# Optimization experiments

Hardware: AMD Instinct MI355X
Metric: run time of the kernel (lower is better)

## Reference

```python
import jax, jax.numpy as jnp
import numpy as np

B, S, D_IN, D_OUT = 4, 2048, 1024, 1024

def setup_inputs() -> dict:
    key = jax.random.key(0)
    k1, k2, k3, k4 = jax.random.split(key, 4)
    x = jax.random.normal(k1, (B, S, D_IN), dtype=jnp.float32)
    # nn.Linear weights: [out, in]; y = x @ W.T
    scale = 1.0 / np.sqrt(D_IN)
    W_key = jax.random.uniform(k2, (D_OUT, D_IN), dtype=jnp.float32, minval=-scale, maxval=scale)
    W_query = jax.random.uniform(k3, (D_OUT, D_IN), dtype=jnp.float32, minval=-scale, maxval=scale)
    W_value = jax.random.uniform(k4, (D_OUT, D_IN), dtype=jnp.float32, minval=-scale, maxval=scale)
    return {"x": x, "W_key": W_key, "W_query": W_query, "W_value": W_value}

def reference(x, W_key, W_query, W_value):
    # x: [B, S, D_IN]; W_*: [D_OUT, D_IN]
    keys = jnp.einsum('bsd,od->bso', x, W_key)
    queries = jnp.einsum('bsd,od->bso', x, W_query)
    values = jnp.einsum('bsd,od->bso', x, W_value)
    # attn_scores: [B, S, S]
    scores = jnp.einsum('bqo,bko->bqk', queries, keys)
    inv_sqrt_d = 1.0 / jnp.sqrt(jnp.asarray(keys.shape[-1], dtype=scores.dtype))
    weights = jax.nn.softmax(scores * inv_sqrt_d, axis=-1)
    context = jnp.einsum('bqk,bko->bqo', weights, values)
    return context
```

## Files before the change

kernel.cpp:

```cpp
#include <hip/hip_runtime.h>

typedef unsigned short u16;
typedef __attribute__((ext_vector_type(4))) float f32x4;
typedef __attribute__((ext_vector_type(8))) short bf16x8;
typedef __attribute__((ext_vector_type(4))) u16 u16x4;
typedef __attribute__((ext_vector_type(8))) u16 u16x8;

__device__ __forceinline__ u16 f2bf(float f) {
    unsigned u = __float_as_uint(f);
    unsigned r = (u + 0x7FFFu + ((u >> 16) & 1u)) >> 16;
    return (u16)r;
}

__device__ __forceinline__ void gld16(const void* g, void* l) {
    __builtin_amdgcn_global_load_lds(
        (const __attribute__((address_space(1))) unsigned*)g,
        (__attribute__((address_space(3))) unsigned*)l,
        16, 0, 0);
}

__global__ __launch_bounds__(256) void cast_kernel(const float* __restrict__ in,
                                                   u16* __restrict__ out, int n4) {
    int i = blockIdx.x * blockDim.x + threadIdx.x;
    int stride = gridDim.x * blockDim.x;
    for (; i < n4; i += stride) {
        f32x4 v = ((const f32x4*)in)[i];
        u16x4 o;
        o[0] = f2bf(v[0]); o[1] = f2bf(v[1]); o[2] = f2bf(v[2]); o[3] = f2bf(v[3]);
        ((u16x4*)out)[i] = o;
    }
}

__global__ __launch_bounds__(256) void zero_kernel(float* __restrict__ p, int n) {
    int i = blockIdx.x * blockDim.x + threadIdx.x;
    if (i < n) p[i] = 0.f;
}

template <int EPI>
__global__ __launch_bounds__(512, 1) void gemm256(
    const u16* __restrict__ A, const u16* __restrict__ Bm, void* __restrict__ Cv,
    int K, int lda, int ldb, int ldc,
    long long sA, long long sB, long long sC, float scale,
    float* __restrict__ denom) {
    extern __shared__ char smem[];
    const u16* Ab = A + (long long)blockIdx.z * sA;
    const u16* Bb = Bm + (long long)blockIdx.z * sB;

    const int tid  = threadIdx.x;
    const int lane = tid & 63;
    const int w    = tid >> 6;
    const int wm   = w >> 2;
    const int wn   = w & 3;
    const int rowBase = blockIdx.x << 8;
    const int colBase = blockIdx.y << 8;
    const int NT = K >> 6;
    const int aRow = lane & 15;

    auto stage = [&](int tile, int h) {
        if (tile >= NT) return;
        const int db = tile & 1;
        const int kt = tile << 6;
        const u16* mat; int ldm, rb, halfRow; char* region;
        if (h == 0)      { mat = Ab; ldm = lda; rb = rowBase; halfRow = 0;   region = smem + db * 32768; }
        else if (h == 1) { mat = Bb; ldm = ldb; rb = colBase; halfRow = 0;   region = smem + 65536 + db * 32768; }
        else if (h == 2) { mat = Bb; ldm = ldb; rb = colBase; halfRow = 128; region = smem + 65536 + db * 32768; }
        else             { mat = Ab; ldm = lda; rb = rowBase; halfRow = 128; region = smem + db * 32768; }
#pragma unroll
        for (int i = 0; i < 2; i++) {
            int o    = ((i * 8 + w) << 10) + lane * 16;
            int r    = o >> 7;
            int slot = (o >> 4) & 7;
            const u16* g = mat + (size_t)(rb + halfRow + r) * ldm + kt +
                           ((slot ^ (r & 7)) << 3);
            gld16(g, region + halfRow * 128 + ((i * 8 + w) << 10));
        }
    };
    auto ldA = [&](int db, int row, int ks) -> bf16x8 {
        int byte = db * 32768 + row * 128 + ((((ks << 2) | (lane >> 4)) ^ (row & 7)) << 4);
        return *(const bf16x8*)(smem + byte);
    };
    auto ldB = [&](int db, int row, int ks) -> bf16x8 {
        int byte = 65536 + db * 32768 + row * 128 + ((((ks << 2) | (lane >> 4)) ^ (row & 7)) << 4);
        return *(const bf16x8*)(smem + byte);
    };

    f32x4 acc[8][4] = {};
    bf16x8 aF[4][2], b0[2][2], b1[2][2];

    stage(0, 0); stage(0, 3); stage(0, 1); stage(0, 2);
    stage(1, 1); stage(1, 2);
    __builtin_amdgcn_sched_barrier(0);
    asm volatile("s_waitcnt vmcnt(4)" ::: "memory");
    __builtin_amdgcn_sched_barrier(0);
    __builtin_amdgcn_s_barrier();

    for (int t = 0; t < NT; ++t) {
        const int db = t & 1;
#pragma unroll
        for (int m = 0; m < 4; m++)
#pragma unroll
            for (int ks = 0; ks < 2; ks++)
                aF[m][ks] = ldA(db, wm * 128 + m * 16 + aRow, ks);
#pragma unroll
        for (int n = 0; n < 2; n++)
#pragma unroll
            for (int ks = 0; ks < 2; ks++)
                b0[n][ks] = ldB(db, wn * 64 + n * 16 + aRow, ks);
        stage(t + 1, 0);
        __builtin_amdgcn_s_barrier();
        asm volatile("s_waitcnt lgkmcnt(0)" ::: "memory");
        __builtin_amdgcn_sched_barrier(0);
        __builtin_amdgcn_s_setprio(1);
#pragma unroll
        for (int ks = 0; ks < 2; ks++)
#pragma unroll
            for (int m = 0; m < 4; m++)
#pragma unroll
                for (int n = 0; n < 2; n++)
                    acc[m][n] = __builtin_amdgcn_mfma_f32_16x16x32_bf16(
                        aF[m][ks], b0[n][ks], acc[m][n], 0, 0, 0);
        __builtin_amdgcn_s_setprio(0);
#pragma unroll
        for (int n = 0; n < 2; n++)
#pragma unroll
            for (int ks = 0; ks < 2; ks++)
                b1[n][ks] = ldB(db, wn * 64 + (n + 2) * 16 + aRow, ks);
        stage(t + 1, 3);
        __builtin_amdgcn_s_barrier();
        asm volatile("s_waitcnt lgkmcnt(0)" ::: "memory");
        __builtin_amdgcn_sched_barrier(0);
        __builtin_amdgcn_s_setprio(1);
#pragma unroll
        for (int ks = 0; ks < 2; ks++)
#pragma unroll
            for (int m = 0; m < 4; m++)
#pragma unroll
                for (int n = 0; n < 2; n++)
                    acc[m][n + 2] = __builtin_amdgcn_mfma_f32_16x16x32_bf16(
                        aF[m][ks], b1[n][ks], acc[m][n + 2], 0, 0, 0);
        __builtin_amdgcn_s_setprio(0);
#pragma unroll
        for (int m = 0; m < 4; m++)
#pragma unroll
            for (int ks = 0; ks < 2; ks++)
                aF[m][ks] = ldA(db, wm * 128 + (m + 4) * 16 + aRow, ks);
        __builtin_amdgcn_s_barrier();
        asm volatile("s_waitcnt lgkmcnt(0)" ::: "memory");
        __builtin_amdgcn_sched_barrier(0);
        __builtin_amdgcn_s_setprio(1);
#pragma unroll
        for (int ks = 0; ks < 2; ks++)
#pragma unroll
            for (int m = 0; m < 4; m++)
#pragma unroll
                for (int n = 0; n < 2; n++)
                    acc[m + 4][n + 2] = __builtin_amdgcn_mfma_f32_16x16x32_bf16(
                        aF[m][ks], b1[n][ks], acc[m + 4][n + 2], 0, 0, 0);
        __builtin_amdgcn_s_setprio(0);
        stage(t + 2, 1);
        stage(t + 2, 2);
        __builtin_amdgcn_sched_barrier(0);
        if (t + 2 < NT) { asm volatile("s_waitcnt vmcnt(4)" ::: "memory"); }
        else            { asm volatile("s_waitcnt vmcnt(0)" ::: "memory"); }
        __builtin_amdgcn_sched_barrier(0);
        __builtin_amdgcn_s_barrier();
        __builtin_amdgcn_s_setprio(1);
#pragma unroll
        for (int ks = 0; ks < 2; ks++)
#pragma unroll
            for (int m = 0; m < 4; m++)
#pragma unroll
                for (int n = 0; n < 2; n++)
                    acc[m + 4][n] = __builtin_amdgcn_mfma_f32_16x16x32_bf16(
                        aF[m][ks], b0[n][ks], acc[m + 4][n], 0, 0, 0);
        __builtin_amdgcn_s_setprio(0);
    }

    const int row0 = rowBase + wm * 128 + ((lane >> 4) << 2);
    const int col0 = colBase + wn * 64 + (lane & 15);
    long long cb = (long long)blockIdx.z * sC;
    if (EPI == 0) {
#pragma unroll
        for (int m = 0; m < 8; m++)
#pragma unroll
            for (int n = 0; n < 4; n++) {
                f32x4 v = acc[m][n];
#pragma unroll
                for (int j = 0; j < 4; j++) {
                    size_t idx = (size_t)(row0 + m * 16 + j) * ldc + (col0 + n * 16);
                    ((u16*)Cv)[cb + idx] = f2bf(v[j] * scale);
                }
            }
    } else {
        float* dz = denom + (long long)blockIdx.z * 2048;
#pragma unroll
        for (int m = 0; m < 8; m++) {
#pragma unroll
            for (int j = 0; j < 4; j++) {
                const int row = row0 + m * 16 + j;
                float rs = 0.f;
#pragma unroll
                for (int n = 0; n < 4; n++) {
                    float e = __expf(fminf(acc[m][n][j] * scale, 60.f));
                    rs += e;
                    ((u16*)Cv)[cb + (size_t)row * ldc + (col0 + n * 16)] = f2bf(e);
                }
#pragma unroll
                for (int off = 1; off < 16; off <<= 1) rs += __shfl_xor(rs, off);
                if ((lane & 15) == 0) atomicAdd(&dz[row], rs);
            }
        }
    }
}

template <int EPI>
__global__ __launch_bounds__(512, 1) void gemm256n128(
    const u16* __restrict__ A, const u16* __restrict__ Bm, void* __restrict__ Cv,
    int K, int lda, int ldb, int ldc,
    long long sA, long long sB, long long sC, float scale,
    const float* __restrict__ denom) {
    extern __shared__ char smem[];
    const u16* Ab = A + (long long)blockIdx.z * sA;
    const u16* Bb = Bm + (long long)blockIdx.z * sB;

    const int tid  = threadIdx.x;
    const int lane = tid & 63;
    const int w    = tid >> 6;
    const int wm   = w >> 1;
    const int wn   = w & 1;
    const int rowBase = blockIdx.x << 8;
    const int colBase = blockIdx.y << 7;
    const int NT = K >> 6;
    const int aRow = lane & 15;

    auto stage = [&](int tile, int h) {
        if (tile >= NT) return;
        const int db = tile & 1;
        const int kt = tile << 6;
        if (h == 0 || h == 3) {
            const int halfRow = (h == 0) ? 0 : 128;
            char* region = smem + db * 32768;
#pragma unroll
            for (int i = 0; i < 2; i++) {
                int o    = i * 8192 + tid * 16;
                int r    = o >> 7;
                int slot = (o >> 4) & 7;
                const u16* g = Ab + (size_t)(rowBase + halfRow + r) * lda + kt +
                               ((slot ^ (r & 7)) << 3);
                gld16(g, region + halfRow * 128 + i * 8192 + (w << 10));
            }
        } else {
            const int halfRow = (h == 1) ? 0 : 64;
            char* region = smem + 65536 + db * 16384;
            int o    = tid * 16;
            int r    = o >> 7;
            int slot = (o >> 4) & 7;
            const u16* g = Bb + (size_t)(colBase + halfRow + r) * ldb + kt +
                           ((slot ^ (r & 7)) << 3);
            gld16(g, region + halfRow * 128 + (w << 10));
        }
    };
    auto ldA = [&](int db, int row, int ks) -> bf16x8 {
        int byte = db * 32768 + row * 128 + ((((ks << 2) | (lane >> 4)) ^ (row & 7)) << 4);
        return *(const bf16x8*)(smem + byte);
    };
    auto ldB = [&](int db, int row, int ks) -> bf16x8 {
        int byte = 65536 + db * 16384 + row * 128 + ((((ks << 2) | (lane >> 4)) ^ (row & 7)) << 4);
        return *(const bf16x8*)(smem + byte);
    };

    f32x4 acc[4][4] = {};
    bf16x8 aF[2][2], b0[2][2], b1[2][2];

    stage(0, 0); stage(0, 3); stage(0, 1); stage(0, 2);
    stage(1, 1); stage(1, 2);
    __builtin_amdgcn_sched_barrier(0);
    asm volatile("s_waitcnt vmcnt(2)" ::: "memory");
    __builtin_amdgcn_sched_barrier(0);
    __builtin_amdgcn_s_barrier();

    for (int t = 0; t < NT; ++t) {
        const int db = t & 1;
#pragma unroll
        for (int m = 0; m < 2; m++)
#pragma unroll
            for (int ks = 0; ks < 2; ks++)
                aF[m][ks] = ldA(db, wm * 64 + m * 16 + aRow, ks);
#pragma unroll
        for (int n = 0; n < 2; n++)
#pragma unroll
            for (int ks = 0; ks < 2; ks++)
                b0[n][ks] = ldB(db, wn * 64 + n * 16 + aRow, ks);
        stage(t + 1, 0);
        __builtin_amdgcn_s_barrier();
        asm volatile("s_waitcnt lgkmcnt(0)" ::: "memory");
        __builtin_amdgcn_sched_barrier(0);
        __builtin_amdgcn_s_setprio(1);
#pragma unroll
        for (int ks = 0; ks < 2; ks++)
#pragma unroll
            for (int m = 0; m < 2; m++)
#pragma unroll
                for (int n = 0; n < 2; n++)
                    acc[m][n] = __builtin_amdgcn_mfma_f32_16x16x32_bf16(
                        aF[m][ks], b0[n][ks], acc[m][n], 0, 0, 0);
        __builtin_amdgcn_s_setprio(0);
#pragma unroll
        for (int n = 0; n < 2; n++)
#pragma unroll
            for (int ks = 0; ks < 2; ks++)
                b1[n][ks] = ldB(db, wn * 64 + (n + 2) * 16 + aRow, ks);
        stage(t + 1, 3);
        __builtin_amdgcn_s_barrier();
        asm volatile("s_waitcnt lgkmcnt(0)" ::: "memory");
        __builtin_amdgcn_sched_barrier(0);
        __builtin_amdgcn_s_setprio(1);
#pragma unroll
        for (int ks = 0; ks < 2; ks++)
#pragma unroll
            for (int m = 0; m < 2; m++)
#pragma unroll
                for (int n = 0; n < 2; n++)
                    acc[m][n + 2] = __builtin_amdgcn_mfma_f32_16x16x32_bf16(
                        aF[m][ks], b1[n][ks], acc[m][n + 2], 0, 0, 0);
        __builtin_amdgcn_s_setprio(0);
#pragma unroll
        for (int m = 0; m < 2; m++)
#pragma unroll
            for (int ks = 0; ks < 2; ks++)
                aF[m][ks] = ldA(db, wm * 64 + (m + 2) * 16 + aRow, ks);
        __builtin_amdgcn_s_barrier();
        asm volatile("s_waitcnt lgkmcnt(0)" ::: "memory");
        __builtin_amdgcn_sched_barrier(0);
        __builtin_amdgcn_s_setprio(1);
#pragma unroll
        for (int ks = 0; ks < 2; ks++)
#pragma unroll
            for (int m = 0; m < 2; m++)
#pragma unroll
                for (int n = 0; n < 2; n++)
                    acc[m + 2][n + 2] = __builtin_amdgcn_mfma_f32_16x16x32_bf16(
                        aF[m][ks], b1[n][ks], acc[m + 2][n + 2], 0, 0, 0);
        __builtin_amdgcn_s_setprio(0);
        stage(t + 2, 1);
        stage(t + 2, 2);
        __builtin_amdgcn_sched_barrier(0);
        if (t + 2 < NT) { asm volatile("s_waitcnt vmcnt(2)" ::: "memory"); }
        else            { asm volatile("s_waitcnt vmcnt(0)" ::: "memory"); }
        __builtin_amdgcn_sched_barrier(0);
        __builtin_amdgcn_s_barrier();
        __builtin_amdgcn_s_setprio(1);
#pragma unroll
        for (int ks = 0; ks < 2; ks++)
#pragma unroll
            for (int m = 0; m < 2; m++)
#pragma unroll
                for (int n = 0; n < 2; n++)
                    acc[m + 2][n] = __builtin_amdgcn_mfma_f32_16x16x32_bf16(
                        aF[m][ks], b0[n][ks], acc[m + 2][n], 0, 0, 0);
        __builtin_amdgcn_s_setprio(0);
    }

    const int row0 = rowBase + wm * 64 + ((lane >> 4) << 2);
    const int col0 = colBase + wn * 64 + (lane & 15);
    long long cb = (long long)blockIdx.z * sC;
    if (EPI == 0) {
#pragma unroll
        for (int m = 0; m < 4; m++)
#pragma unroll
            for (int n = 0; n < 4; n++) {
                f32x4 v = acc[m][n];
#pragma unroll
                for (int j = 0; j < 4; j++) {
                    size_t idx = (size_t)(row0 + m * 16 + j) * ldc + (col0 + n * 16);
                    ((u16*)Cv)[cb + idx] = f2bf(v[j] * scale);
                }
            }
    } else {
        const float* dz = denom + (long long)blockIdx.z * 2048;
        float inv[4][4];
#pragma unroll
        for (int m = 0; m < 4; m++)
#pragma unroll
            for (int j = 0; j < 4; j++)
                inv[m][j] = 1.0f / dz[row0 + m * 16 + j];
#pragma unroll
        for (int m = 0; m < 4; m++)
#pragma unroll
            for (int n = 0; n < 4; n++) {
                f32x4 v = acc[m][n];
#pragma unroll
                for (int j = 0; j < 4; j++) {
                    size_t idx = (size_t)(row0 + m * 16 + j) * ldc + (col0 + n * 16);
                    ((float*)Cv)[cb + idx] = v[j] * inv[m][j];
                }
            }
    }
}

extern "C" void kernel_launch(void* const* d_in, const int* in_sizes, int n_in,
                              void* d_out, int out_size, void* d_ws, size_t ws_size,
                              hipStream_t stream) {
    const float* x  = (const float*)d_in[0];
    const float* Wk = (const float*)d_in[1];
    const float* Wq = (const float*)d_in[2];
    const float* Wv = (const float*)d_in[3];
    float* out = (float*)d_out;
    char* ws = (char*)d_ws;
    const size_t MB = 1u << 20;

    u16* xb    = (u16*)(ws);
    u16* Wqk   = (u16*)(ws + 16 * MB);
    u16* Wvb   = (u16*)(ws + 20 * MB);
    float* den = (float*)(ws + 22 * MB);
    u16* QK    = (u16*)(ws + 64 * MB);
    u16* VT    = (u16*)(ws + 96 * MB);
    u16* Pb    = (u16*)(ws + 112 * MB);

    const long long SS = 2048LL * 2048;

    hipFuncSetAttribute((const void*)gemm256<0>, hipFuncAttributeMaxDynamicSharedMemorySize, 131072);
    hipFuncSetAttribute((const void*)gemm256<2>, hipFuncAttributeMaxDynamicSharedMemorySize, 131072);
    hipFuncSetAttribute((const void*)gemm256n128<0>, hipFuncAttributeMaxDynamicSharedMemorySize, 98304);
    hipFuncSetAttribute((const void*)gemm256n128<3>, hipFuncAttributeMaxDynamicSharedMemorySize, 98304);

    cast_kernel<<<2048, 256, 0, stream>>>(x, xb, 8388608 / 4);
    cast_kernel<<<1024, 256, 0, stream>>>(Wq, Wqk, 1048576 / 4);
    cast_kernel<<<1024, 256, 0, stream>>>(Wk, Wqk + 1048576, 1048576 / 4);
    cast_kernel<<<1024, 256, 0, stream>>>(Wv, Wvb, 1048576 / 4);
    zero_kernel<<<32, 256, 0, stream>>>(den, 8192);

    gemm256<0><<<dim3(32, 8, 1), 512, 131072, stream>>>(
        xb, Wqk, QK, 1024, 1024, 1024, 2048, 0, 0, 0, 1.0f, nullptr);
    gemm256n128<0><<<dim3(4, 64, 1), 512, 98304, stream>>>(
        Wvb, xb, VT, 1024, 1024, 1024, 8192, 0, 0, 0, 1.0f, nullptr);
    gemm256<2><<<dim3(8, 8, 4), 512, 131072, stream>>>(
        QK, QK + 1024, Pb, 1024, 2048, 2048, 2048, SS, SS, SS, 0.03125f, den);
    gemm256n128<3><<<dim3(8, 8, 4), 512, 98304, stream>>>(
        Pb, VT, out, 2048, 2048, 8192, 1024, SS, 2048LL, 2048LL * 1024, 1.0f, den);
}
```

Baseline: 156.8 us.

## Software-pipeline LDS fragment loads across MFMA quadrants with separate register sets

```diff
diff --git a/kernel.cpp b/kernel.cpp
--- a/kernel.cpp
+++ b/kernel.cpp
@@ -85,7 +85,7 @@
     };
 
     f32x4 acc[8][4] = {};
-    bf16x8 aF[4][2], b0[2][2], b1[2][2];
+    bf16x8 a01[4][2], a23[4][2], b01[2][2], b23[2][2];
 
     stage(0, 0); stage(0, 3); stage(0, 1); stage(0, 2);
     stage(1, 1); stage(1, 2);
@@ -93,20 +93,56 @@
     asm volatile("s_waitcnt vmcnt(4)" ::: "memory");
     __builtin_amdgcn_sched_barrier(0);
     __builtin_amdgcn_s_barrier();
+#pragma unroll
+    for (int m = 0; m < 4; m++)
+#pragma unroll
+        for (int ks = 0; ks < 2; ks++)
+            a01[m][ks] = ldA(0, wm * 128 + m * 16 + aRow, ks);
+#pragma unroll
+    for (int n = 0; n < 2; n++)
+#pragma unroll
+        for (int ks = 0; ks < 2; ks++)
+            b01[n][ks] = ldB(0, wn * 64 + n * 16 + aRow, ks);
 
     for (int t = 0; t < NT; ++t) {
         const int db = t & 1;
 #pragma unroll
+        for (int n = 0; n < 2; n++)
+#pragma unroll
+            for (int ks = 0; ks < 2; ks++)
+                b23[n][ks] = ldB(db, wn * 64 + (n + 2) * 16 + aRow, ks);
+        stage(t + 1, 0);
+        asm volatile("s_waitcnt lgkmcnt(4)" ::: "memory");
+        __builtin_amdgcn_sched_barrier(0);
+        __builtin_amdgcn_s_setprio(1);
+#pragma unroll
+        for (int ks = 0; ks < 2; ks++)
+#pragma unroll
+            for (int m = 0; m < 4; m++)
+#pragma unroll
+                for (int n = 0; n < 2; n++)
+                    acc[m][n] = __builtin_amdgcn_mfma_f32_16x16x32_bf16(
+                        a01[m][ks], b01[n][ks], acc[m][n], 0, 0, 0);
+        __builtin_amdgcn_s_setprio(0);
+        __builtin_amdgcn_s_barrier();
+#pragma unroll
         for (int m = 0; m < 4; m++)
 #pragma unroll
             for (int ks = 0; ks < 2; ks++)
-                aF[m][ks] = ldA(db, wm * 128 + m * 16 + aRow, ks);
-#pragma unroll
-        for (int n = 0; n < 2; n++)
-#pragma unroll
-            for (int ks = 0; ks < 2; ks++)
-                b0[n][ks] = ldB(db, wn * 64 + n * 16 + aRow, ks);
-        stage(t + 1, 0);
+                a23[m][ks] = ldA(db, wm * 128 + (m + 4) * 16 + aRow, ks);
+        stage(t + 1, 3);
+        asm volatile("s_waitcnt lgkmcnt(8)" ::: "memory");
+        __builtin_amdgcn_sched_barrier(0);
+        __builtin_amdgcn_s_setprio(1);
+#pragma unroll
+        for (int ks = 0; ks < 2; ks++)
+#pragma unroll
+            for (int m = 0; m < 4; m++)
+#pragma unroll
+                for (int n = 0; n < 2; n++)
+                    acc[m][n + 2] = __builtin_amdgcn_mfma_f32_16x16x32_bf16(
+                        a01[m][ks], b23[n][ks], acc[m][n + 2], 0, 0, 0);
+        __builtin_amdgcn_s_setprio(0);
         __builtin_amdgcn_s_barrier();
         asm volatile("s_waitcnt lgkmcnt(0)" ::: "memory");
         __builtin_amdgcn_sched_barrier(0);
@@ -117,46 +153,10 @@
             for (int m = 0; m < 4; m++)
 #pragma unroll
                 for (int n = 0; n < 2; n++)
-                    acc[m][n] = __builtin_amdgcn_mfma_f32_16x16x32_bf16(
-                        aF[m][ks], b0[n][ks], acc[m][n], 0, 0, 0);
-        __builtin_amdgcn_s_setprio(0);
-#pragma unroll
-        for (int n = 0; n < 2; n++)
-#pragma unroll
-            for (int ks = 0; ks < 2; ks++)
-                b1[n][ks] = ldB(db, wn * 64 + (n + 2) * 16 + aRow, ks);
-        stage(t + 1, 3);
-        __builtin_amdgcn_s_barrier();
-        asm volatile("s_waitcnt lgkmcnt(0)" ::: "memory");
-        __builtin_amdgcn_sched_barrier(0);
-        __builtin_amdgcn_s_setprio(1);
-#pragma unroll
-        for (int ks = 0; ks < 2; ks++)
-#pragma unroll
-            for (int m = 0; m < 4; m++)
-#pragma unroll
-                for (int n = 0; n < 2; n++)
-                    acc[m][n + 2] = __builtin_amdgcn_mfma_f32_16x16x32_bf16(
-                        aF[m][ks], b1[n][ks], acc[m][n + 2], 0, 0, 0);
-        __builtin_amdgcn_s_setprio(0);
-#pragma unroll
-        for (int m = 0; m < 4; m++)
-#pragma unroll
-            for (int ks = 0; ks < 2; ks++)
-                aF[m][ks] = ldA(db, wm * 128 + (m + 4) * 16 + aRow, ks);
-        __builtin_amdgcn_s_barrier();
-        asm volatile("s_waitcnt lgkmcnt(0)" ::: "memory");
-        __builtin_amdgcn_sched_barrier(0);
-        __builtin_amdgcn_s_setprio(1);
-#pragma unroll
-        for (int ks = 0; ks < 2; ks++)
-#pragma unroll
-            for (int m = 0; m < 4; m++)
-#pragma unroll
-                for (int n = 0; n < 2; n++)
-                    acc[m + 4][n + 2] = __builtin_amdgcn_mfma_f32_16x16x32_bf16(
-                        aF[m][ks], b1[n][ks], acc[m + 4][n + 2], 0, 0, 0);
-        __builtin_amdgcn_s_setprio(0);
+                    acc[m + 4][n] = __builtin_amdgcn_mfma_f32_16x16x32_bf16(
+                        a23[m][ks], b01[n][ks], acc[m + 4][n], 0, 0, 0);
+        __builtin_amdgcn_s_setprio(0);
+        __builtin_amdgcn_s_barrier();
         stage(t + 2, 1);
         stage(t + 2, 2);
         __builtin_amdgcn_sched_barrier(0);
@@ -164,15 +164,28 @@
         else            { asm volatile("s_waitcnt vmcnt(0)" ::: "memory"); }
         __builtin_amdgcn_sched_barrier(0);
         __builtin_amdgcn_s_barrier();
-        __builtin_amdgcn_s_setprio(1);
-#pragma unroll
-        for (int ks = 0; ks < 2; ks++)
+        if (t + 1 < NT) {
 #pragma unroll
             for (int m = 0; m < 4; m++)
 #pragma unroll
-                for (int n = 0; n < 2; n++)
-                    acc[m + 4][n] = __builtin_amdgcn_mfma_f32_16x16x32_bf16(
-                        aF[m][ks], b0[n][ks], acc[m + 4][n], 0, 0, 0);
+                for (int ks = 0; ks < 2; ks++)
+                    a01[m][ks] = ldA(db ^ 1, wm * 128 + m * 16 + aRow, ks);
+#pragma unroll
+            for (int n = 0; n < 2; n++)
+#pragma unroll
+                for (int ks = 0; ks < 2; ks++)
+                    b01[n][ks] = ldB(db ^ 1, wn * 64 + n * 16 + aRow, ks);
+        }
+        __builtin_amdgcn_sched_barrier(0);
+        __builtin_amdgcn_s_setprio(1);
+#pragma unroll
+        for (int ks = 0; ks < 2; ks++)
+#pragma unroll
+            for (int m = 0; m < 4; m++)
+#pragma unroll
+                for (int n = 0; n < 2; n++)
+                    acc[m + 4][n + 2] = __builtin_amdgcn_mfma_f32_16x16x32_bf16(
+                        a23[m][ks], b23[n][ks], acc[m + 4][n + 2], 0, 0, 0);
         __builtin_amdgcn_s_setprio(0);
     }
 
@@ -270,7 +283,7 @@
     };
 
     f32x4 acc[4][4] = {};
-    bf16x8 aF[2][2], b0[2][2], b1[2][2];
+    bf16x8 a01[2][2], a23[2][2], b01[2][2], b23[2][2];
 
     stage(0, 0); stage(0, 3); stage(0, 1); stage(0, 2);
     stage(1, 1); stage(1, 2);
@@ -278,20 +291,56 @@
     asm volatile("s_waitcnt vmcnt(2)" ::: "memory");
     __builtin_amdgcn_sched_barrier(0);
     __builtin_amdgcn_s_barrier();
+#pragma unroll
+    for (int m = 0; m < 2; m++)
+#pragma unroll
+        for (int ks = 0; ks < 2; ks++)
+            a01[m][ks] = ldA(0, wm * 64 + m * 16 + aRow, ks);
+#pragma unroll
+    for (int n = 0; n < 2; n++)
+#pragma unroll
+        for (int ks = 0; ks < 2; ks++)
+            b01[n][ks] = ldB(0, wn * 64 + n * 16 + aRow, ks);
 
     for (int t = 0; t < NT; ++t) {
         const int db = t & 1;
 #pragma unroll
+        for (int n = 0; n < 2; n++)
+#pragma unroll
+            for (int ks = 0; ks < 2; ks++)
+                b23[n][ks] = ldB(db, wn * 64 + (n + 2) * 16 + aRow, ks);
+        stage(t + 1, 0);
+        asm volatile("s_waitcnt lgkmcnt(4)" ::: "memory");
+        __builtin_amdgcn_sched_barrier(0);
+        __builtin_amdgcn_s_setprio(1);
+#pragma unroll
+        for (int ks = 0; ks < 2; ks++)
+#pragma unroll
+            for (int m = 0; m < 2; m++)
+#pragma unroll
+                for (int n = 0; n < 2; n++)
+                    acc[m][n] = __builtin_amdgcn_mfma_f32_16x16x32_bf16(
+                        a01[m][ks], b01[n][ks], acc[m][n], 0, 0, 0);
+        __builtin_amdgcn_s_setprio(0);
+        __builtin_amdgcn_s_barrier();
+#pragma unroll
         for (int m = 0; m < 2; m++)
 #pragma unroll
             for (int ks = 0; ks < 2; ks++)
-                aF[m][ks] = ldA(db, wm * 64 + m * 16 + aRow, ks);
-#pragma unroll
-        for (int n = 0; n < 2; n++)
-#pragma unroll
-            for (int ks = 0; ks < 2; ks++)
-                b0[n][ks] = ldB(db, wn * 64 + n * 16 + aRow, ks);
-        stage(t + 1, 0);
+                a23[m][ks] = ldA(db, wm * 64 + (m + 2) * 16 + aRow, ks);
+        stage(t + 1, 3);
+        asm volatile("s_waitcnt lgkmcnt(4)" ::: "memory");
+        __builtin_amdgcn_sched_barrier(0);
+        __builtin_amdgcn_s_setprio(1);
+#pragma unroll
+        for (int ks = 0; ks < 2; ks++)
+#pragma unroll
+            for (int m = 0; m < 2; m++)
+#pragma unroll
+                for (int n = 0; n < 2; n++)
+                    acc[m][n + 2] = __builtin_amdgcn_mfma_f32_16x16x32_bf16(
+                        a01[m][ks], b23[n][ks], acc[m][n + 2], 0, 0, 0);
+        __builtin_amdgcn_s_setprio(0);
         __builtin_amdgcn_s_barrier();
         asm volatile("s_waitcnt lgkmcnt(0)" ::: "memory");
         __builtin_amdgcn_sched_barrier(0);
@@ -302,46 +351,10 @@
             for (int m = 0; m < 2; m++)
 #pragma unroll
                 for (int n = 0; n < 2; n++)
-                    acc[m][n] = __builtin_amdgcn_mfma_f32_16x16x32_bf16(
-                        aF[m][ks], b0[n][ks], acc[m][n], 0, 0, 0);
-        __builtin_amdgcn_s_setprio(0);
-#pragma unroll
-        for (int n = 0; n < 2; n++)
-#pragma unroll
-            for (int ks = 0; ks < 2; ks++)
-                b1[n][ks] = ldB(db, wn * 64 + (n + 2) * 16 + aRow, ks);
-        stage(t + 1, 3);
-        __builtin_amdgcn_s_barrier();
-        asm volatile("s_waitcnt lgkmcnt(0)" ::: "memory");
-        __builtin_amdgcn_sched_barrier(0);
-        __builtin_amdgcn_s_setprio(1);
-#pragma unroll
-        for (int ks = 0; ks < 2; ks++)
-#pragma unroll
-            for (int m = 0; m < 2; m++)
-#pragma unroll
-                for (int n = 0; n < 2; n++)
-                    acc[m][n + 2] = __builtin_amdgcn_mfma_f32_16x16x32_bf16(
-                        aF[m][ks], b1[n][ks], acc[m][n + 2], 0, 0, 0);
-        __builtin_amdgcn_s_setprio(0);
-#pragma unroll
-        for (int m = 0; m < 2; m++)
-#pragma unroll
-            for (int ks = 0; ks < 2; ks++)
-                aF[m][ks] = ldA(db, wm * 64 + (m + 2) * 16 + aRow, ks);
-        __builtin_amdgcn_s_barrier();
-        asm volatile("s_waitcnt lgkmcnt(0)" ::: "memory");
-        __builtin_amdgcn_sched_barrier(0);
-        __builtin_amdgcn_s_setprio(1);
-#pragma unroll
-        for (int ks = 0; ks < 2; ks++)
-#pragma unroll
-            for (int m = 0; m < 2; m++)
-#pragma unroll
-                for (int n = 0; n < 2; n++)
-                    acc[m + 2][n + 2] = __builtin_amdgcn_mfma_f32_16x16x32_bf16(
-                        aF[m][ks], b1[n][ks], acc[m + 2][n + 2], 0, 0, 0);
-        __builtin_amdgcn_s_setprio(0);
+                    acc[m + 2][n] = __builtin_amdgcn_mfma_f32_16x16x32_bf16(
+                        a23[m][ks], b01[n][ks], acc[m + 2][n], 0, 0, 0);
+        __builtin_amdgcn_s_setprio(0);
+        __builtin_amdgcn_s_barrier();
         stage(t + 2, 1);
         stage(t + 2, 2);
         __builtin_amdgcn_sched_barrier(0);
@@ -349,15 +362,28 @@
         else            { asm volatile("s_waitcnt vmcnt(0)" ::: "memory"); }
         __builtin_amdgcn_sched_barrier(0);
         __builtin_amdgcn_s_barrier();
-        __builtin_amdgcn_s_setprio(1);
-#pragma unroll
-        for (int ks = 0; ks < 2; ks++)
+        if (t + 1 < NT) {
 #pragma unroll
             for (int m = 0; m < 2; m++)
 #pragma unroll
-                for (int n = 0; n < 2; n++)
-                    acc[m + 2][n] = __builtin_amdgcn_mfma_f32_16x16x32_bf16(
-                        aF[m][ks], b0[n][ks], acc[m + 2][n], 0, 0, 0);
+                for (int ks = 0; ks < 2; ks++)
+                    a01[m][ks] = ldA(db ^ 1, wm * 64 + m * 16 + aRow, ks);
+#pragma unroll
+            for (int n = 0; n < 2; n++)
+#pragma unroll
+                for (int ks = 0; ks < 2; ks++)
+                    b01[n][ks] = ldB(db ^ 1, wn * 64 + n * 16 + aRow, ks);
+        }
+        __builtin_amdgcn_sched_barrier(0);
+        __builtin_amdgcn_s_setprio(1);
+#pragma unroll
+        for (int ks = 0; ks < 2; ks++)
+#pragma unroll
+            for (int m = 0; m < 2; m++)
+#pragma unroll
+                for (int n = 0; n < 2; n++)
+                    acc[m + 2][n + 2] = __builtin_amdgcn_mfma_f32_16x16x32_bf16(
+                        a23[m][ks], b23[n][ks], acc[m + 2][n + 2], 0, 0, 0);
         __builtin_amdgcn_s_setprio(0);
     }
 
```

Result: no change. 159.8 us (+1.9%).

## Fuse QKV projections into one GEMM and remap blocks across XCDs

Applied to the files above, without the earlier changes.

```diff
diff --git a/kernel.cpp b/kernel.cpp
--- a/kernel.cpp
+++ b/kernel.cpp
@@ -17,6 +17,17 @@
         (const __attribute__((address_space(1))) unsigned*)g,
         (__attribute__((address_space(3))) unsigned*)l,
         16, 0, 0);
+}
+
+__device__ __forceinline__ void xcd_map(int& bx, int& by, int& bz) {
+    const int gx = gridDim.x, gxy = gridDim.x * gridDim.y;
+    const int F = blockIdx.x + gx * (blockIdx.y + gridDim.y * blockIdx.z);
+    const int cpx = (gxy * gridDim.z) >> 3;
+    const int L = (F & 7) * cpx + (F >> 3);
+    bz = L / gxy;
+    const int r = L % gxy;
+    by = r / gx;
+    bx = r % gx;
 }
 
 __global__ __launch_bounds__(256) void cast_kernel(const float* __restrict__ in,
@@ -41,18 +52,20 @@
     const u16* __restrict__ A, const u16* __restrict__ Bm, void* __restrict__ Cv,
     int K, int lda, int ldb, int ldc,
     long long sA, long long sB, long long sC, float scale,
-    float* __restrict__ denom) {
+    float* __restrict__ denom, u16* __restrict__ vt) {
     extern __shared__ char smem[];
-    const u16* Ab = A + (long long)blockIdx.z * sA;
-    const u16* Bb = Bm + (long long)blockIdx.z * sB;
+    int bx, by, bz;
+    xcd_map(bx, by, bz);
+    const u16* Ab = A + (long long)bz * sA;
+    const u16* Bb = Bm + (long long)bz * sB;
 
     const int tid  = threadIdx.x;
     const int lane = tid & 63;
     const int w    = tid >> 6;
     const int wm   = w >> 2;
     const int wn   = w & 3;
-    const int rowBase = blockIdx.x << 8;
-    const int colBase = blockIdx.y << 8;
+    const int rowBase = bx << 8;
+    const int colBase = by << 8;
     const int NT = K >> 6;
     const int aRow = lane & 15;
 
@@ -178,21 +191,35 @@
 
     const int row0 = rowBase + wm * 128 + ((lane >> 4) << 2);
     const int col0 = colBase + wn * 64 + (lane & 15);
-    long long cb = (long long)blockIdx.z * sC;
-    if (EPI == 0) {
-#pragma unroll
-        for (int m = 0; m < 8; m++)
-#pragma unroll
-            for (int n = 0; n < 4; n++) {
-                f32x4 v = acc[m][n];
-#pragma unroll
-                for (int j = 0; j < 4; j++) {
-                    size_t idx = (size_t)(row0 + m * 16 + j) * ldc + (col0 + n * 16);
-                    ((u16*)Cv)[cb + idx] = f2bf(v[j] * scale);
+    long long cb = (long long)bz * sC;
+    if (EPI == 1) {
+        if (colBase < 2048) {
+#pragma unroll
+            for (int m = 0; m < 8; m++)
+#pragma unroll
+                for (int n = 0; n < 4; n++) {
+                    f32x4 v = acc[m][n];
+#pragma unroll
+                    for (int j = 0; j < 4; j++) {
+                        size_t idx = (size_t)(row0 + m * 16 + j) * ldc + (col0 + n * 16);
+                        ((u16*)Cv)[idx] = f2bf(v[j]);
+                    }
                 }
-            }
+        } else {
+#pragma unroll
+            for (int m = 0; m < 8; m++)
+#pragma unroll
+                for (int n = 0; n < 4; n++) {
+                    f32x4 v = acc[m][n];
+                    u16x4 o4;
+#pragma unroll
+                    for (int j = 0; j < 4; j++) o4[j] = f2bf(v[j]);
+                    *(u16x4*)(vt + (size_t)(col0 + n * 16 - 2048) * 8192 +
+                              (row0 + m * 16)) = o4;
+                }
+        }
     } else {
-        float* dz = denom + (long long)blockIdx.z * 2048;
+        float* dz = denom + (long long)bz * 2048;
 #pragma unroll
         for (int m = 0; m < 8; m++) {
 #pragma unroll
@@ -220,16 +247,18 @@
     long long sA, long long sB, long long sC, float scale,
     const float* __restrict__ denom) {
     extern __shared__ char smem[];
-    const u16* Ab = A + (long long)blockIdx.z * sA;
-    const u16* Bb = Bm + (long long)blockIdx.z * sB;
+    int bx, by, bz;
+    xcd_map(bx, by, bz);
+    const u16* Ab = A + (long long)bz * sA;
+    const u16* Bb = Bm + (long long)bz * sB;
 
     const int tid  = threadIdx.x;
     const int lane = tid & 63;
     const int w    = tid >> 6;
     const int wm   = w >> 1;
     const int wn   = w & 1;
-    const int rowBase = blockIdx.x << 8;
-    const int colBase = blockIdx.y << 7;
+    const int rowBase = bx << 8;
+    const int colBase = by << 7;
     const int NT = K >> 6;
     const int aRow = lane & 15;
 
@@ -363,7 +392,7 @@
 
     const int row0 = rowBase + wm * 64 + ((lane >> 4) << 2);
     const int col0 = colBase + wn * 64 + (lane & 15);
-    long long cb = (long long)blockIdx.z * sC;
+    long long cb = (long long)bz * sC;
     if (EPI == 0) {
 #pragma unroll
         for (int m = 0; m < 4; m++)
@@ -377,7 +406,7 @@
                 }
             }
     } else {
-        const float* dz = denom + (long long)blockIdx.z * 2048;
+        const float* dz = denom + (long long)bz * 2048;
         float inv[4][4];
 #pragma unroll
         for (int m = 0; m < 4; m++)
@@ -410,32 +439,28 @@
     const size_t MB = 1u << 20;
 
     u16* xb    = (u16*)(ws);
-    u16* Wqk   = (u16*)(ws + 16 * MB);
-    u16* Wvb   = (u16*)(ws + 20 * MB);
-    float* den = (float*)(ws + 22 * MB);
+    u16* Wqkv  = (u16*)(ws + 16 * MB);
+    float* den = (float*)(ws + 24 * MB);
     u16* QK    = (u16*)(ws + 64 * MB);
     u16* VT    = (u16*)(ws + 96 * MB);
     u16* Pb    = (u16*)(ws + 112 * MB);
 
     const long long SS = 2048LL * 2048;
 
-    hipFuncSetAttribute((const void*)gemm256<0>, hipFuncAttributeMaxDynamicSharedMemorySize, 131072);
+    hipFuncSetAttribute((const void*)gemm256<1>, hipFuncAttributeMaxDynamicSharedMemorySize, 131072);
     hipFuncSetAttribute((const void*)gemm256<2>, hipFuncAttributeMaxDynamicSharedMemorySize, 131072);
-    hipFuncSetAttribute((const void*)gemm256n128<0>, hipFuncAttributeMaxDynamicSharedMemorySize, 98304);
     hipFuncSetAttribute((const void*)gemm256n128<3>, hipFuncAttributeMaxDynamicSharedMemorySize, 98304);
 
     cast_kernel<<<2048, 256, 0, stream>>>(x, xb, 8388608 / 4);
-    cast_kernel<<<1024, 256, 0, stream>>>(Wq, Wqk, 1048576 / 4);
-    cast_kernel<<<1024, 256, 0, stream>>>(Wk, Wqk + 1048576, 1048576 / 4);
-    cast_kernel<<<1024, 256, 0, stream>>>(Wv, Wvb, 1048576 / 4);
+    cast_kernel<<<1024, 256, 0, stream>>>(Wq, Wqkv, 1048576 / 4);
+    cast_kernel<<<1024, 256, 0, stream>>>(Wk, Wqkv + 1048576, 1048576 / 4);
+    cast_kernel<<<1024, 256, 0, stream>>>(Wv, Wqkv + 2097152, 1048576 / 4);
     zero_kernel<<<32, 256, 0, stream>>>(den, 8192);
 
-    gemm256<0><<<dim3(32, 8, 1), 512, 131072, stream>>>(
-        xb, Wqk, QK, 1024, 1024, 1024, 2048, 0, 0, 0, 1.0f, nullptr);
-    gemm256n128<0><<<dim3(4, 64, 1), 512, 98304, stream>>>(
-        Wvb, xb, VT, 1024, 1024, 1024, 8192, 0, 0, 0, 1.0f, nullptr);
+    gemm256<1><<<dim3(32, 12, 1), 512, 131072, stream>>>(
+        xb, Wqkv, QK, 1024, 1024, 1024, 2048, 0, 0, 0, 1.0f, nullptr, VT);
     gemm256<2><<<dim3(8, 8, 4), 512, 131072, stream>>>(
-        QK, QK + 1024, Pb, 1024, 2048, 2048, 2048, SS, SS, SS, 0.03125f, den);
+        QK, QK + 1024, Pb, 1024, 2048, 2048, 2048, SS, SS, SS, 0.03125f, den, nullptr);
     gemm256n128<3><<<dim3(8, 8, 4), 512, 98304, stream>>>(
         Pb, VT, out, 2048, 2048, 8192, 1024, SS, 2048LL, 2048LL * 1024, 1.0f, den);
 }
```

Measured after the change: 161.9 us. +3.2%, slower.
